# Kernel optimization log

Measured on AMD Instinct MI355X. Metric: run time of the kernel, lower is better.

The kernel has to match this reference:

```python
import jax, jax.numpy as jnp
import numpy as np

B, L, D, M, S = 1024, 50, 64, 100000, 2
NEG = float(-2**32 + 1)

def _ln(x):
    # F.layer_norm over last dim, no affine, eps=1e-8 (biased variance)
    mu = x.mean(-1, keepdims=True)
    var = ((x - mu) ** 2).mean(-1, keepdims=True)
    return (x - mu) / jnp.sqrt(var + 1e-8)

def setup_inputs():
    key = jax.random.key(0)
    ks = jax.random.split(key, 24)
    p = lambda i, shape: jax.random.normal(ks[i], shape, jnp.float32) * 0.05
    return {
        'user_items': jax.random.randint(ks[0], (B, L), 0, M + 1),
        'pos_items': jax.random.randint(ks[1], (B, L), 0, M + 1),
        'neg_items': jax.random.randint(ks[2], (B, L), 0, M + 1),
        'padding_mask': jnp.ones((B, L, 1), jnp.float32),
        'item_embedding': p(3, (M + 1, D)),
        'pos_embedding': p(4, (L, D)),
        'Q_sabs': p(5, (S, D, D)),
        'K_sabs': p(6, (S, D, D)),
        'V_sabs': p(7, (S, D, D)),
        'c1_w': p(8, (S, L, L)), 'c1_b': p(9, (S, L)),
        'c2_w': p(10, (S, L, L)), 'c2_b': p(11, (S, L)),
        'query_item': p(12, (1, 1, D)),
        'K_lba': p(13, (D, D)), 'V_lba': p(14, (D, D)),
        'l1_w': p(15, (1, 1)), 'l1_b': p(16, (1,)),
        'l2_w': p(17, (1, 1)), 'l2_b': p(18, (1,)),
        'gated_weight': p(19, (3 * D, 1)),
        'gated_bias': p(20, (1, 1)),
    }

def _forward(user_items, pos_items, neg_items, padding_mask, item_embedding,
             pos_embedding, Q_sabs, K_sabs, V_sabs, c1_w, c1_b, c2_w, c2_b,
             query_item, K_lba, V_lba, l1_w, l1_b, l2_w, l2_b,
             gated_weight, gated_bias):
    ie = item_embedding[user_items]                      # [B,L,D]
    inputs = ie + pos_embedding[None]                    # add positional (dropout = identity)
    inputs = inputs * padding_mask
    inputs = _ln(inputs)

    tril = jnp.tril(jnp.ones((L, L), inputs.dtype))
    key_mask = jnp.transpose(padding_mask, (0, 2, 1))    # [B,1,L]
    scale = D ** 0.5

    x = inputs
    for i in range(S):
        Qx = x @ Q_sabs[i]; Kx = x @ K_sabs[i]; Vx = x @ V_sabs[i]
        scores = jnp.einsum('bqd,bkd->bqk', Qx, Kx) / scale      # [B,L,L]
        scores = jnp.where(tril[None] == 0, NEG, scores)          # causal mask
        scores = jnp.where(key_mask == 0, NEG, scores)            # key padding mask
        scores = scores * padding_mask                            # query mask (NO softmax, as in source)
        att = jnp.einsum('bqk,bkd->bqd', scores, Vx) + x          # residual
        att = _ln(att)
        # Conv1d(L, L, 1) mixes across the sequence-position axis
        h = jax.nn.relu(jnp.einsum('ij,bjd->bid', c1_w[i], att) + c1_b[i][None, :, None])
        ff = jnp.einsum('ij,bjd->bid', c2_w[i], h) + c2_b[i][None, :, None] + att
        ff = ff * padding_mask
        x = _ln(ff)
    loc = x                                                       # [B,L,D]

    # location-based attention: single learned query over sequence
    Kx = inputs @ K_lba; Vx = inputs @ V_lba
    sc = jnp.einsum('qd,bld->bql', query_item[0], Kx)             # [B,1,L]
    sc = jnp.where(key_mask == 0, NEG, sc)
    sc = jax.nn.softmax(sc, axis=-1)
    glo = jnp.einsum('bql,bld->bqd', sc, Vx)                      # [B,1,D]
    glo = _ln(glo)
    h = jax.nn.relu(l1_w[0, 0] * glo + l1_b[0])                   # Conv1d(1,1,1) = scalar affine
    glo = l2_w[0, 0] * h + l2_b[0] + glo
    glo = _ln(glo)

    pos_e = item_embedding[pos_items]                             # [B,L,D]
    neg_e = item_embedding[neg_items]
    ms = jnp.concatenate([ie, ie], 0)                             # tile [2,1,1]
    y = jnp.tile(glo, (2, L, 1))                                  # [2B,L,D]
    mi = jnp.concatenate([pos_e, neg_e], 0)
    cat = jnp.concatenate([ms, y, mi], -1).reshape(-1, 3 * D)
    logits = (cat @ gated_weight + gated_bias).reshape(2 * B, L, 1)
    gating = jax.nn.sigmoid(jax.nn.sigmoid(logits))               # double sigmoid, as in source

    tl = jnp.concatenate([loc, loc], 0)
    tg = jnp.tile(glo, (2, 1, 1))
    out = tl * gating + tg * (1.0 - gating)
    out = out * jnp.concatenate([padding_mask, padding_mask], 0)
    out = _ln(out)
    op, on = out[:B], out[B:]
    return jnp.stack([jnp.sum(op * pos_e, -1), jnp.sum(on * neg_e, -1)], 0)  # [2,B,L]

def reference(user_items, pos_items, neg_items, padding_mask, item_embedding,
              pos_embedding, Q_sabs, K_sabs, V_sabs, c1_w, c1_b, c2_w, c2_b,
              query_item, K_lba, V_lba, l1_w, l1_b, l2_w, l2_b,
              gated_weight, gated_bias):
    return _forward(user_items, pos_items, neg_items, padding_mask, item_embedding,
                    pos_embedding, Q_sabs, K_sabs, V_sabs, c1_w, c1_b, c2_w, c2_b,
                    query_item, K_lba, V_lba, l1_w, l1_b, l2_w, l2_b,
                    gated_weight, gated_bias)
```

## Files before the change

### kernel.cpp

```cpp
#include <hip/hip_runtime.h>


#define NB 1024
#define LL 50
#define DD 64
#define LD 66
#define LDC 51
#define NR 7
#define NEGV (-4294967295.0f)

__device__ __forceinline__ float wsum(float v) {
#pragma unroll
  for (int m = 32; m >= 1; m >>= 1) v += __shfl_xor(v, m, 64);
  return v;
}
__device__ __forceinline__ float wmax(float v) {
#pragma unroll
  for (int m = 32; m >= 1; m >>= 1) v = fmaxf(v, __shfl_xor(v, m, 64));
  return v;
}
__device__ __forceinline__ float rowln(float v) {
  float m = wsum(v) * (1.f / 64.f);
  float df = v - m;
  float var = wsum(df * df) * (1.f / 64.f);
  return df / sqrtf(var + 1e-8f);
}

__global__ __launch_bounds__(512, 1) void fissa_kernel(
    const int* __restrict__ user_items, const int* __restrict__ pos_items,
    const int* __restrict__ neg_items, const float* __restrict__ pmask,
    const float* __restrict__ item_emb, const float* __restrict__ pos_emb,
    const float* __restrict__ Qs, const float* __restrict__ Ks,
    const float* __restrict__ Vs, const float* __restrict__ c1w,
    const float* __restrict__ c1b, const float* __restrict__ c2w,
    const float* __restrict__ c2b, const float* __restrict__ query,
    const float* __restrict__ Klba, const float* __restrict__ Vlba,
    const float* __restrict__ l1w, const float* __restrict__ l1b,
    const float* __restrict__ l2w, const float* __restrict__ l2b,
    const float* __restrict__ gw, const float* __restrict__ gb,
    float* __restrict__ out) {
  __shared__ float s_in[LL * LD];
  __shared__ float s_x[LL * LD];
  __shared__ float s_a[LL * LD];
  __shared__ float s_b[LL * LD];
  __shared__ float s_c[LL * LDC];
  __shared__ float s_mask[64], s_bias[64], s_qv[64], s_glo[64], s_gw[192], s_scal[2];

  const int b = blockIdx.x;
  const int tid = threadIdx.x;
  const int wv = tid >> 6, ln = tid & 63;

  int qrow[NR];
  int qoff[NR];
  int coff[NR];
  bool qok[NR];
#pragma unroll
  for (int r = 0; r < NR; ++r) {
    int q = wv + 8 * r;
    qok[r] = (q < LL);
    qrow[r] = qok[r] ? q : (LL - 1);
    qoff[r] = qrow[r] * LD;
    coff[r] = qrow[r] * LDC;
  }

  if (tid < 64) s_mask[tid] = (tid < LL) ? pmask[b * LL + tid] : 0.f;
  else if (tid < 128) s_qv[tid - 64] = query[tid - 64];
  else if (tid < 320) s_gw[tid - 128] = gw[tid - 128];

#pragma unroll
  for (int r = 0; r < NR; ++r) {
    int l = qrow[r];
    int u = user_items[b * LL + l];
    float mk = pmask[b * LL + l];
    float v = (item_emb[(size_t)u * DD + ln] + pos_emb[l * DD + ln]) * mk;
    float o = rowln(v);
    if (qok[r]) { s_in[qoff[r] + ln] = o; s_x[qoff[r] + ln] = o; }
  }
  __syncthreads();

  for (int i = 0; i < 2; ++i) {
    const float* Qc = Qs + i * DD * DD + ln;
    const float* Kc = Ks + i * DD * DD + ln;
    const float* Vc = Vs + i * DD * DD + ln;

    {
      float aq[NR], ak[NR];
#pragma unroll
      for (int r = 0; r < NR; ++r) { aq[r] = 0.f; ak[r] = 0.f; }
#pragma unroll 4
      for (int k = 0; k < DD; ++k) {
        float wq = Qc[k * DD];
        float wk = Kc[k * DD];
#pragma unroll
        for (int r = 0; r < NR; ++r) {
          float xv = s_x[qoff[r] + k];
          aq[r] = fmaf(xv, wq, aq[r]);
          ak[r] = fmaf(xv, wk, ak[r]);
        }
      }
#pragma unroll
      for (int r = 0; r < NR; ++r)
        if (qok[r]) { s_a[qoff[r] + ln] = aq[r]; s_b[qoff[r] + ln] = ak[r]; }
    }
    __syncthreads();

    {
      float sc[NR];
#pragma unroll
      for (int r = 0; r < NR; ++r) sc[r] = 0.f;
      const int kk = (ln < LL) ? ln : (LL - 1);
      const float* krow = &s_b[kk * LD];
#pragma unroll 4
      for (int d = 0; d < DD; ++d) {
        float kv = krow[d];
#pragma unroll
        for (int r = 0; r < NR; ++r)
          sc[r] = fmaf(s_a[qoff[r] + d], kv, sc[r]);
      }
      if (ln < LL) {
        float mk = s_mask[ln];
#pragma unroll
        for (int r = 0; r < NR; ++r)
          if (qok[r]) {
            float v = sc[r] * 0.125f;
            if (ln > qrow[r]) v = NEGV;
            if (mk == 0.f) v = NEGV;
            v *= s_mask[qrow[r]];
            s_c[coff[r] + ln] = v;
          }
      }
    }
    __syncthreads();

    {
      float av[NR];
#pragma unroll
      for (int r = 0; r < NR; ++r) av[r] = 0.f;
#pragma unroll 4
      for (int k = 0; k < DD; ++k) {
        float wvv = Vc[k * DD];
#pragma unroll
        for (int r = 0; r < NR; ++r)
          av[r] = fmaf(s_x[qoff[r] + k], wvv, av[r]);
      }
#pragma unroll
      for (int r = 0; r < NR; ++r)
        if (qok[r]) s_a[qoff[r] + ln] = av[r];
    }
    __syncthreads();

    {
      float at[NR];
#pragma unroll
      for (int r = 0; r < NR; ++r) at[r] = s_x[qoff[r] + ln];
#pragma unroll 2
      for (int k = 0; k < LL; ++k) {
        float vv = s_a[k * LD + ln];
#pragma unroll
        for (int r = 0; r < NR; ++r)
          at[r] = fmaf(s_c[coff[r] + k], vv, at[r]);
      }
#pragma unroll
      for (int r = 0; r < NR; ++r) {
        float o = rowln(at[r]);
        if (qok[r]) s_x[qoff[r] + ln] = o;
      }
    }
    __syncthreads();

    for (int e = tid; e < LL * LL; e += 512) {
      int q = e / LL;
      s_c[q * LDC + (e - q * LL)] = c1w[i * LL * LL + e];
    }
    if (tid < LL) s_bias[tid] = c1b[i * LL + tid];
    __syncthreads();

    {
      float hh[NR];
#pragma unroll
      for (int r = 0; r < NR; ++r) hh[r] = 0.f;
#pragma unroll 2
      for (int j = 0; j < LL; ++j) {
        float xv = s_x[j * LD + ln];
#pragma unroll
        for (int r = 0; r < NR; ++r)
          hh[r] = fmaf(s_c[coff[r] + j], xv, hh[r]);
      }
#pragma unroll
      for (int r = 0; r < NR; ++r)
        if (qok[r]) s_b[qoff[r] + ln] = fmaxf(hh[r] + s_bias[qrow[r]], 0.f);
    }
    __syncthreads();

    for (int e = tid; e < LL * LL; e += 512) {
      int q = e / LL;
      s_c[q * LDC + (e - q * LL)] = c2w[i * LL * LL + e];
    }
    if (tid < LL) s_bias[tid] = c2b[i * LL + tid];
    __syncthreads();

    {
      float f0[NR];
#pragma unroll
      for (int r = 0; r < NR; ++r) f0[r] = s_x[qoff[r] + ln];
#pragma unroll 2
      for (int j = 0; j < LL; ++j) {
        float hv = s_b[j * LD + ln];
#pragma unroll
        for (int r = 0; r < NR; ++r)
          f0[r] = fmaf(s_c[coff[r] + j], hv, f0[r]);
      }
#pragma unroll
      for (int r = 0; r < NR; ++r) {
        float v = (f0[r] + s_bias[qrow[r]]) * s_mask[qrow[r]];
        float o = rowln(v);
        if (qok[r]) s_x[qoff[r] + ln] = o;
      }
    }
    __syncthreads();
  }

  {
    float akl[NR], avl[NR];
#pragma unroll
    for (int r = 0; r < NR; ++r) { akl[r] = 0.f; avl[r] = 0.f; }
    const float* Kc = Klba + ln;
    const float* Vc = Vlba + ln;
#pragma unroll 4
    for (int k = 0; k < DD; ++k) {
      float wk = Kc[k * DD];
      float wvv = Vc[k * DD];
#pragma unroll
      for (int r = 0; r < NR; ++r) {
        float xv = s_in[qoff[r] + k];
        akl[r] = fmaf(xv, wk, akl[r]);
        avl[r] = fmaf(xv, wvv, avl[r]);
      }
    }
#pragma unroll
    for (int r = 0; r < NR; ++r)
      if (qok[r]) { s_a[qoff[r] + ln] = akl[r]; s_b[qoff[r] + ln] = avl[r]; }
  }
  __syncthreads();

  if (wv == 0) {
    float sc = -INFINITY;
    if (ln < LL) {
      float acc = 0.f;
#pragma unroll
      for (int d = 0; d < DD; ++d) acc += s_qv[d] * s_a[ln * LD + d];
      sc = acc;
      if (s_mask[ln] == 0.f) sc = NEGV;
    }
    float mx = wmax(sc);
    float e = (ln < LL) ? expf(sc - mx) : 0.f;
    float den = wsum(e);
    if (ln < LL) s_bias[ln] = e / den;
    float acc = 0.f;
#pragma unroll
    for (int l = 0; l < LL; ++l) acc += s_bias[l] * s_b[l * LD + ln];
    float g = rowln(acc);
    float w1 = l1w[0], bb1 = l1b[0], w2 = l2w[0], bb2 = l2b[0];
    float h = fmaxf(w1 * g + bb1, 0.f);
    float glo = rowln(w2 * h + bb2 + g);
    s_glo[ln] = glo;
    float gs = wsum(glo * s_gw[64 + ln]);
    if (ln == 0) s_scal[0] = gs + gb[0];
  }
  __syncthreads();

  float g2c = s_scal[0];
  float gloc = s_glo[ln];
  for (int row = wv; row < 2 * LL; row += 8) {
    int sgn = row >= LL;
    int l = row - sgn * LL;
    int u = user_items[b * LL + l];
    int it = sgn ? neg_items[b * LL + l] : pos_items[b * LL + l];
    float ie_d = item_emb[(size_t)u * DD + ln];
    float mi_d = item_emb[(size_t)it * DD + ln];
    float logit = wsum(ie_d * s_gw[ln] + mi_d * s_gw[128 + ln]) + g2c;
    float sg = 1.f / (1.f + expf(-logit));
    float g = 1.f / (1.f + expf(-sg));
    float od = (s_x[l * LD + ln] * g + gloc * (1.f - g)) * s_mask[l];
    float o = rowln(od);
    float res = wsum(o * mi_d);
    if (ln == 0) out[(sgn * NB + b) * LL + l] = res;
  }
}

extern "C" void kernel_launch(void* const* d_in, const int* in_sizes, int n_in,
                              void* d_out, int out_size, void* d_ws, size_t ws_size,
                              hipStream_t stream) {
  const int* user_items = (const int*)d_in[0];
  const int* pos_items = (const int*)d_in[1];
  const int* neg_items = (const int*)d_in[2];
  const float* pmask = (const float*)d_in[3];
  const float* item_emb = (const float*)d_in[4];
  const float* pos_emb = (const float*)d_in[5];
  const float* Qs = (const float*)d_in[6];
  const float* Ks = (const float*)d_in[7];
  const float* Vs = (const float*)d_in[8];
  const float* c1w = (const float*)d_in[9];
  const float* c1b = (const float*)d_in[10];
  const float* c2w = (const float*)d_in[11];
  const float* c2b = (const float*)d_in[12];
  const float* query = (const float*)d_in[13];
  const float* Klba = (const float*)d_in[14];
  const float* Vlba = (const float*)d_in[15];
  const float* l1w = (const float*)d_in[16];
  const float* l1b = (const float*)d_in[17];
  const float* l2w = (const float*)d_in[18];
  const float* l2b = (const float*)d_in[19];
  const float* gw = (const float*)d_in[20];
  const float* gb = (const float*)d_in[21];
  float* out = (float*)d_out;

  fissa_kernel<<<dim3(NB), dim3(512), 0, stream>>>(
      user_items, pos_items, neg_items, pmask, item_emb, pos_emb, Qs, Ks, Vs,
      c1w, c1b, c2w, c2b, query, Klba, Vlba, l1w, l1b, l2w, l2b, gw, gb, out);
}
```

Measured before the change: 402.1 us.

## Vectorize LDS reads as float2, reorder global branch first, drop s_in buffer

Moves the global (LBA) attention branch ahead of the self-attention loop so it reads the initial embeddings from s_x. This lets the separate s_in shared buffer be dropped, cutting LDS use so more blocks can be resident, and launch bounds now request 6 blocks per CU. All inner GEMM-like loops are rewritten to consume two k values per iteration through float2 LDS loads, which halves LDS load instructions. LDC becomes 52 so that the s_c rows stay 8-byte aligned for the float2 reads. The gain depends on occupancy actually rising, and the tighter launch bound may force register spills.

```diff
diff --git a/kernel.cpp b/kernel.cpp
--- a/kernel.cpp
+++ b/kernel.cpp
@@ -5,7 +5,7 @@
 #define LL 50
 #define DD 64
 #define LD 66
-#define LDC 51
+#define LDC 52
 #define NR 7
 #define NEGV (-4294967295.0f)
 
@@ -25,8 +25,11 @@
   float var = wsum(df * df) * (1.f / 64.f);
   return df / sqrtf(var + 1e-8f);
 }
-
-__global__ __launch_bounds__(512, 1) void fissa_kernel(
+__device__ __forceinline__ float2 ld2(const float* p) {
+  return *reinterpret_cast<const float2*>(p);
+}
+
+__global__ __launch_bounds__(512, 6) void fissa_kernel(
     const int* __restrict__ user_items, const int* __restrict__ pos_items,
     const int* __restrict__ neg_items, const float* __restrict__ pmask,
     const float* __restrict__ item_emb, const float* __restrict__ pos_emb,
@@ -39,7 +42,6 @@
     const float* __restrict__ l2w, const float* __restrict__ l2b,
     const float* __restrict__ gw, const float* __restrict__ gb,
     float* __restrict__ out) {
-  __shared__ float s_in[LL * LD];
   __shared__ float s_x[LL * LD];
   __shared__ float s_a[LL * LD];
   __shared__ float s_b[LL * LD];
@@ -50,9 +52,7 @@
   const int tid = threadIdx.x;
   const int wv = tid >> 6, ln = tid & 63;
 
-  int qrow[NR];
-  int qoff[NR];
-  int coff[NR];
+  int qrow[NR], qoff[NR], coff[NR];
   bool qok[NR];
 #pragma unroll
   for (int r = 0; r < NR; ++r) {
@@ -74,7 +74,61 @@
     float mk = pmask[b * LL + l];
     float v = (item_emb[(size_t)u * DD + ln] + pos_emb[l * DD + ln]) * mk;
     float o = rowln(v);
-    if (qok[r]) { s_in[qoff[r] + ln] = o; s_x[qoff[r] + ln] = o; }
+    if (qok[r]) s_x[qoff[r] + ln] = o;
+  }
+  __syncthreads();
+
+  {
+    float akl[NR], avl[NR];
+#pragma unroll
+    for (int r = 0; r < NR; ++r) { akl[r] = 0.f; avl[r] = 0.f; }
+    const float* Kc = Klba + ln;
+    const float* Vc = Vlba + ln;
+#pragma unroll 2
+    for (int k = 0; k < DD; k += 2) {
+      float wk0 = Kc[k * DD], wk1 = Kc[(k + 1) * DD];
+      float wv0 = Vc[k * DD], wv1 = Vc[(k + 1) * DD];
+#pragma unroll
+      for (int r = 0; r < NR; ++r) {
+        float2 xv = ld2(&s_x[qoff[r] + k]);
+        akl[r] = fmaf(xv.x, wk0, akl[r]);
+        akl[r] = fmaf(xv.y, wk1, akl[r]);
+        avl[r] = fmaf(xv.x, wv0, avl[r]);
+        avl[r] = fmaf(xv.y, wv1, avl[r]);
+      }
+    }
+#pragma unroll
+    for (int r = 0; r < NR; ++r)
+      if (qok[r]) { s_a[qoff[r] + ln] = akl[r]; s_b[qoff[r] + ln] = avl[r]; }
+  }
+  __syncthreads();
+  if (wv == 0) {
+    float sc = -INFINITY;
+    if (ln < LL) {
+      float acc = 0.f;
+      const float* arow = &s_a[ln * LD];
+#pragma unroll
+      for (int d = 0; d < DD; d += 2) {
+        float2 av = ld2(&arow[d]);
+        acc = fmaf(s_qv[d], av.x, acc);
+        acc = fmaf(s_qv[d + 1], av.y, acc);
+      }
+      sc = acc;
+      if (s_mask[ln] == 0.f) sc = NEGV;
+    }
+    float mx = wmax(sc);
+    float e = (ln < LL) ? expf(sc - mx) : 0.f;
+    float den = wsum(e);
+    if (ln < LL) s_bias[ln] = e / den;
+    float acc = 0.f;
+#pragma unroll 2
+    for (int l = 0; l < LL; ++l) acc = fmaf(s_bias[l], s_b[l * LD + ln], acc);
+    float g = rowln(acc);
+    float h = fmaxf(l1w[0] * g + l1b[0], 0.f);
+    float glo = rowln(l2w[0] * h + l2b[0] + g);
+    s_glo[ln] = glo;
+    float gs = wsum(glo * s_gw[64 + ln]);
+    if (ln == 0) s_scal[0] = gs + gb[0];
   }
   __syncthreads();
 
@@ -87,15 +141,17 @@
       float aq[NR], ak[NR];
 #pragma unroll
       for (int r = 0; r < NR; ++r) { aq[r] = 0.f; ak[r] = 0.f; }
-#pragma unroll 4
-      for (int k = 0; k < DD; ++k) {
-        float wq = Qc[k * DD];
-        float wk = Kc[k * DD];
-#pragma unroll
-        for (int r = 0; r < NR; ++r) {
-          float xv = s_x[qoff[r] + k];
-          aq[r] = fmaf(xv, wq, aq[r]);
-          ak[r] = fmaf(xv, wk, ak[r]);
+#pragma unroll 2
+      for (int k = 0; k < DD; k += 2) {
+        float wq0 = Qc[k * DD], wq1 = Qc[(k + 1) * DD];
+        float wk0 = Kc[k * DD], wk1 = Kc[(k + 1) * DD];
+#pragma unroll
+        for (int r = 0; r < NR; ++r) {
+          float2 xv = ld2(&s_x[qoff[r] + k]);
+          aq[r] = fmaf(xv.x, wq0, aq[r]);
+          aq[r] = fmaf(xv.y, wq1, aq[r]);
+          ak[r] = fmaf(xv.x, wk0, ak[r]);
+          ak[r] = fmaf(xv.y, wk1, ak[r]);
         }
       }
 #pragma unroll
@@ -110,12 +166,15 @@
       for (int r = 0; r < NR; ++r) sc[r] = 0.f;
       const int kk = (ln < LL) ? ln : (LL - 1);
       const float* krow = &s_b[kk * LD];
-#pragma unroll 4
-      for (int d = 0; d < DD; ++d) {
-        float kv = krow[d];
-#pragma unroll
-        for (int r = 0; r < NR; ++r)
-          sc[r] = fmaf(s_a[qoff[r] + d], kv, sc[r]);
+#pragma unroll 2
+      for (int d = 0; d < DD; d += 2) {
+        float2 kv = ld2(&krow[d]);
+#pragma unroll
+        for (int r = 0; r < NR; ++r) {
+          float2 qv = ld2(&s_a[qoff[r] + d]);
+          sc[r] = fmaf(qv.x, kv.x, sc[r]);
+          sc[r] = fmaf(qv.y, kv.y, sc[r]);
+        }
       }
       if (ln < LL) {
         float mk = s_mask[ln];
@@ -136,12 +195,15 @@
       float av[NR];
 #pragma unroll
       for (int r = 0; r < NR; ++r) av[r] = 0.f;
-#pragma unroll 4
-      for (int k = 0; k < DD; ++k) {
-        float wvv = Vc[k * DD];
-#pragma unroll
-        for (int r = 0; r < NR; ++r)
-          av[r] = fmaf(s_x[qoff[r] + k], wvv, av[r]);
+#pragma unroll 2
+      for (int k = 0; k < DD; k += 2) {
+        float wv0 = Vc[k * DD], wv1 = Vc[(k + 1) * DD];
+#pragma unroll
+        for (int r = 0; r < NR; ++r) {
+          float2 xv = ld2(&s_x[qoff[r] + k]);
+          av[r] = fmaf(xv.x, wv0, av[r]);
+          av[r] = fmaf(xv.y, wv1, av[r]);
+        }
       }
 #pragma unroll
       for (int r = 0; r < NR; ++r)
@@ -154,11 +216,15 @@
 #pragma unroll
       for (int r = 0; r < NR; ++r) at[r] = s_x[qoff[r] + ln];
 #pragma unroll 2
-      for (int k = 0; k < LL; ++k) {
-        float vv = s_a[k * LD + ln];
-#pragma unroll
-        for (int r = 0; r < NR; ++r)
-          at[r] = fmaf(s_c[coff[r] + k], vv, at[r]);
+      for (int k = 0; k < LL; k += 2) {
+        float v0 = s_a[k * LD + ln];
+        float v1 = s_a[(k + 1) * LD + ln];
+#pragma unroll
+        for (int r = 0; r < NR; ++r) {
+          float2 sv = ld2(&s_c[coff[r] + k]);
+          at[r] = fmaf(sv.x, v0, at[r]);
+          at[r] = fmaf(sv.y, v1, at[r]);
+        }
       }
 #pragma unroll
       for (int r = 0; r < NR; ++r) {
@@ -180,11 +246,15 @@
 #pragma unroll
       for (int r = 0; r < NR; ++r) hh[r] = 0.f;
 #pragma unroll 2
-      for (int j = 0; j < LL; ++j) {
-        float xv = s_x[j * LD + ln];
-#pragma unroll
-        for (int r = 0; r < NR; ++r)
-          hh[r] = fmaf(s_c[coff[r] + j], xv, hh[r]);
+      for (int j = 0; j < LL; j += 2) {
+        float x0 = s_x[j * LD + ln];
+        float x1 = s_x[(j + 1) * LD + ln];
+#pragma unroll
+        for (int r = 0; r < NR; ++r) {
+          float2 cv = ld2(&s_c[coff[r] + j]);
+          hh[r] = fmaf(cv.x, x0, hh[r]);
+          hh[r] = fmaf(cv.y, x1, hh[r]);
+        }
       }
 #pragma unroll
       for (int r = 0; r < NR; ++r)
@@ -204,11 +274,15 @@
 #pragma unroll
       for (int r = 0; r < NR; ++r) f0[r] = s_x[qoff[r] + ln];
 #pragma unroll 2
-      for (int j = 0; j < LL; ++j) {
-        float hv = s_b[j * LD + ln];
-#pragma unroll
-        for (int r = 0; r < NR; ++r)
-          f0[r] = fmaf(s_c[coff[r] + j], hv, f0[r]);
+      for (int j = 0; j < LL; j += 2) {
+        float h0 = s_b[j * LD + ln];
+        float h1 = s_b[(j + 1) * LD + ln];
+#pragma unroll
+        for (int r = 0; r < NR; ++r) {
+          float2 cv = ld2(&s_c[coff[r] + j]);
+          f0[r] = fmaf(cv.x, h0, f0[r]);
+          f0[r] = fmaf(cv.y, h1, f0[r]);
+        }
       }
 #pragma unroll
       for (int r = 0; r < NR; ++r) {
@@ -219,55 +293,6 @@
     }
     __syncthreads();
   }
-
-  {
-    float akl[NR], avl[NR];
-#pragma unroll
-    for (int r = 0; r < NR; ++r) { akl[r] = 0.f; avl[r] = 0.f; }
-    const float* Kc = Klba + ln;
-    const float* Vc = Vlba + ln;
-#pragma unroll 4
-    for (int k = 0; k < DD; ++k) {
-      float wk = Kc[k * DD];
-      float wvv = Vc[k * DD];
-#pragma unroll
-      for (int r = 0; r < NR; ++r) {
-        float xv = s_in[qoff[r] + k];
-        akl[r] = fmaf(xv, wk, akl[r]);
-        avl[r] = fmaf(xv, wvv, avl[r]);
-      }
-    }
-#pragma unroll
-    for (int r = 0; r < NR; ++r)
-      if (qok[r]) { s_a[qoff[r] + ln] = akl[r]; s_b[qoff[r] + ln] = avl[r]; }
-  }
-  __syncthreads();
-
-  if (wv == 0) {
-    float sc = -INFINITY;
-    if (ln < LL) {
-      float acc = 0.f;
-#pragma unroll
-      for (int d = 0; d < DD; ++d) acc += s_qv[d] * s_a[ln * LD + d];
-      sc = acc;
-      if (s_mask[ln] == 0.f) sc = NEGV;
-    }
-    float mx = wmax(sc);
-    float e = (ln < LL) ? expf(sc - mx) : 0.f;
-    float den = wsum(e);
-    if (ln < LL) s_bias[ln] = e / den;
-    float acc = 0.f;
-#pragma unroll
-    for (int l = 0; l < LL; ++l) acc += s_bias[l] * s_b[l * LD + ln];
-    float g = rowln(acc);
-    float w1 = l1w[0], bb1 = l1b[0], w2 = l2w[0], bb2 = l2b[0];
-    float h = fmaxf(w1 * g + bb1, 0.f);
-    float glo = rowln(w2 * h + bb2 + g);
-    s_glo[ln] = glo;
-    float gs = wsum(glo * s_gw[64 + ln]);
-    if (ln == 0) s_scal[0] = gs + gb[0];
-  }
-  __syncthreads();
 
   float g2c = s_scal[0];
   float gloc = s_glo[ln];
```

Result: no change. 408.4 us (+1.6%).
